# Optimization experiments

Measured on AMD Instinct MI355X. Metric: run time of the kernel, lower is better.

## Reference

```python
import jax, jax.numpy as jnp
import numpy as np

B, T, E, H, D = 2, 2048, 1024, 16, 64  # D = attention_dim // num_heads

def setup_inputs() -> dict:
    key = jax.random.key(0)
    k1, k2, k3, k4 = jax.random.split(key, 4)
    scale = 1.0 / np.sqrt(E)  # ~ torch Linear init scale
    embedded = jax.random.normal(k1, (B, T, E), dtype=jnp.float32)
    Wq = jax.random.normal(k2, (H, D, E), dtype=jnp.float32) * scale
    Wk = jax.random.normal(k3, (H, D, E), dtype=jnp.float32) * scale
    Wv = jax.random.normal(k4, (H, D, E), dtype=jnp.float32) * scale
    return {"embedded": embedded, "Wq": Wq, "Wk": Wk, "Wv": Wv}

def reference(embedded, Wq, Wk, Wv):
    # Batched multi-head projection (original loops per head; same math).
    q = jnp.einsum('bte,hde->bhtd', embedded, Wq)
    k = jnp.einsum('bte,hde->bhtd', embedded, Wk)
    v = jnp.einsum('bte,hde->bhtd', embedded, Wv)
    scores = jnp.einsum('bhtd,bhsd->bhts', q, k) / jnp.sqrt(jnp.float32(D))
    causal = jnp.tril(jnp.ones((T, T), dtype=bool))  # [T,T]
    scores = jnp.where(causal, scores, -jnp.inf)
    attn = jax.nn.softmax(scores, axis=-1)
    out = jnp.einsum('bhts,bhsd->bhtd', attn, v)
    # concat heads on last dim: [B,T,H*D]
    return out.transpose(0, 2, 1, 3).reshape(B, T, H * D)
```

## Files before the change

kernel.cpp:

```cpp
#include <hip/hip_runtime.h>
#include <hip/hip_bf16.h>
#include <stdint.h>

typedef __bf16 bf16_t;
typedef __bf16 bf16x4 __attribute__((ext_vector_type(4)));
typedef __bf16 bf16x8 __attribute__((ext_vector_type(8)));
typedef float  f32x4  __attribute__((ext_vector_type(4)));

#define QK_SCALE 0.1803368801111204f

__device__ __forceinline__ void gload_lds16(const void* g, void* l) {
    __builtin_amdgcn_global_load_lds(
        (__attribute__((address_space(1))) unsigned int*)(uintptr_t)g,
        (__attribute__((address_space(3))) unsigned int*)(uint32_t)(uintptr_t)l,
        16, 0, 0);
}

__global__ __launch_bounds__(256) void convert_kernel(
    const float* __restrict__ emb, const float* __restrict__ wq,
    const float* __restrict__ wk,  const float* __restrict__ wv,
    bf16_t* __restrict__ embb, bf16_t* __restrict__ wcat)
{
    size_t base = ((size_t)blockIdx.x * 256 + threadIdx.x) * 8;
    const float* src;
    bf16_t* dst;
    if (base < (size_t)4194304) { src = emb + base; dst = embb + base; }
    else {
        size_t r = base - 4194304;
        int wsel = (int)(r >> 20);
        size_t off = r & 1048575;
        src = (wsel == 0 ? wq : (wsel == 1 ? wk : wv)) + off;
        dst = wcat + r;
    }
    float4 a  = *(const float4*)src;
    float4 c2 = *(const float4*)(src + 4);
    bf16x8 o;
    o[0]=(bf16_t)a.x;  o[1]=(bf16_t)a.y;  o[2]=(bf16_t)a.z;  o[3]=(bf16_t)a.w;
    o[4]=(bf16_t)c2.x; o[5]=(bf16_t)c2.y; o[6]=(bf16_t)c2.z; o[7]=(bf16_t)c2.w;
    *(bf16x8*)dst = o;
}

__global__ __launch_bounds__(256, 3) void proj_kernel(
    const bf16_t* __restrict__ A, const bf16_t* __restrict__ Wc,
    bf16_t* __restrict__ qo, bf16_t* __restrict__ ko, bf16_t* __restrict__ vto)
{
    __shared__ __align__(128) char smem[49152];

    const int tid  = threadIdx.x;
    const int w    = tid >> 6, lane = tid & 63;
    const int wr   = w >> 1,  wc2  = w & 1;
    const int g    = lane >> 4, c = lane & 15;
    const int bm   = blockIdx.x & 31, bn = blockIdx.x >> 5;
    const int m0   = bm * 128, n0 = bn * 128;

    f32x4 acc[4][4] = {};

    const int arow = lane >> 2;
    const int acol = (((lane & 3) ^ ((lane >> 3) & 3))) * 8;

    #define PROJ_STAGE(buf, kt)                                                        \
        do {                                                                           \
            char* As_ = smem + (buf) * 16384;                                          \
            char* Bs_ = As_ + 8192;                                                    \
            _Pragma("unroll")                                                          \
            for (int p = 0; p < 2; ++p) {                                              \
                gload_lds16(A  + (size_t)(m0 + p*64 + w*16 + arow) * 1024 + (kt)*32 + acol, \
                            As_ + (p*64 + w*16) * 64);                                 \
                gload_lds16(Wc + (size_t)(n0 + p*64 + w*16 + arow) * 1024 + (kt)*32 + acol, \
                            Bs_ + (p*64 + w*16) * 64);                                 \
            }                                                                          \
        } while (0)

    PROJ_STAGE(0, 0);
    PROJ_STAGE(1, 1);
    int cur = 0;
    for (int kt = 0; kt < 32; ++kt) {
        if (kt == 31) asm volatile("s_waitcnt vmcnt(0)" ::: "memory");
        else          asm volatile("s_waitcnt vmcnt(4)" ::: "memory");
        __builtin_amdgcn_s_barrier();
        asm volatile("" ::: "memory");
        if (kt + 2 < 32) {
            int b2 = cur + 2; if (b2 >= 3) b2 -= 3;
            PROJ_STAGE(b2, kt + 2);
        }
        const char* As = smem + cur * 16384;
        const char* Bs = As + 8192;
        const int sw = (c >> 1) & 3;
        bf16x8 af[4], bf[4];
        #pragma unroll
        for (int i = 0; i < 4; ++i) {
            af[i] = *(const bf16x8*)(As + (wr*64  + i*16 + c) * 64 + ((g ^ sw) << 4));
            bf[i] = *(const bf16x8*)(Bs + (wc2*64 + i*16 + c) * 64 + ((g ^ sw) << 4));
        }
        #pragma unroll
        for (int i = 0; i < 4; ++i)
            #pragma unroll
            for (int j = 0; j < 4; ++j)
                acc[i][j] = __builtin_amdgcn_mfma_f32_16x16x32_bf16(af[i], bf[j], acc[i][j], 0, 0, 0);
        cur = (cur == 2) ? 0 : cur + 1;
    }
    __syncthreads();

    const int b  = m0 >> 11;
    const int t0 = m0 & 2047;

    if (n0 < 2048) {
        bf16_t* dst = (n0 < 1024) ? qo : ko;
        const int nl0 = n0 & 1023;
        #pragma unroll
        for (int i = 0; i < 4; ++i)
            #pragma unroll
            for (int j = 0; j < 4; ++j) {
                int dl = wc2*64 + j*16 + c;
                #pragma unroll
                for (int e = 0; e < 4; ++e) {
                    int tl = wr*64 + i*16 + g*4 + e;
                    *(bf16_t*)(smem + ((tl*256 + dl*2) ^ ((tl & 7) << 4))) = (bf16_t)acc[i][j][e];
                }
            }
        __syncthreads();
        #pragma unroll
        for (int it = 0; it < 8; ++it) {
            int chunk = it * 256 + tid;
            int tl = chunk >> 4;
            int ce = (chunk & 15) * 8;
            bf16x8 val = *(const bf16x8*)(smem + ((tl*256 + ce*2) ^ ((tl & 7) << 4)));
            int nn = nl0 + ce;
            int hh = nn >> 6, dd = nn & 63;
            *(bf16x8*)(dst + ((size_t)(b*16 + hh) * 2048 + (t0 + tl)) * 64 + dd) = val;
        }
    } else {
        #pragma unroll
        for (int i = 0; i < 4; ++i)
            #pragma unroll
            for (int j = 0; j < 4; ++j) {
                int dl = wc2*64 + j*16 + c;
                #pragma unroll
                for (int e = 0; e < 4; ++e) {
                    int tl = wr*64 + i*16 + g*4 + e;
                    *(bf16_t*)(smem + ((dl*256 + tl*2) ^ ((dl & 7) << 4))) = (bf16_t)acc[i][j][e];
                }
            }
        __syncthreads();
        const int nvbase = n0 - 2048;
        #pragma unroll
        for (int it = 0; it < 8; ++it) {
            int chunk = it * 256 + tid;
            int dl = chunk >> 4;
            int tc = (chunk & 15) * 8;
            bf16x8 val = *(const bf16x8*)(smem + ((dl*256 + tc*2) ^ ((dl & 7) << 4)));
            int nv = nvbase + dl;
            int hh = nv >> 6, dd = nv & 63;
            *(bf16x8*)(vto + (size_t)((b*16 + hh)*64 + dd) * 2048 + t0 + tc) = val;
        }
    }
    #undef PROJ_STAGE
}

__global__ __launch_bounds__(256, 3) void attn_kernel(
    const bf16_t* __restrict__ qg, const bf16_t* __restrict__ kg,
    const bf16_t* __restrict__ vtg, float* __restrict__ out)
{
    __shared__ __align__(128) char smem[49152];

    const int tid = threadIdx.x;
    const int w = tid >> 6, lane = tid & 63;
    const int g = lane >> 4, c = lane & 15;
    const int id = blockIdx.x;
    const int qt = 31 - (id >> 5);
    const int bh = id & 31;
    const int b = bh >> 4, h = bh & 15;

    const bf16_t* qbase = qg  + (size_t)bh * 2048 * 64;
    const bf16_t* kbase = kg  + (size_t)bh * 2048 * 64;
    const bf16_t* vbase = vtg + (size_t)bh * 64 * 2048;
    float* obase = out + (size_t)b * 2048 * 1024 + h * 64;

    const int srow = lane >> 3;
    const int scol = ((lane & 7) ^ srow) * 8;

    const int q0 = qt * 64;
    const int nt = qt + 1;

    bf16x8 qf[2];
    #pragma unroll
    for (int kf = 0; kf < 2; ++kf) {
        bf16x8 v = *(const bf16x8*)(qbase + (size_t)(q0 + w*16 + c) * 64 + kf*32 + g*8);
        #pragma unroll
        for (int e = 0; e < 8; ++e) qf[kf][e] = (bf16_t)((float)v[e] * QK_SCALE);
    }

    f32x4 oacc[4] = {};
    float mrun = -INFINITY, lrun = 0.0f;

    #define ATTN_STAGE(buf, kt)                                                          \
        do {                                                                             \
            char* Kb_ = smem + (buf) * 16384;                                            \
            _Pragma("unroll")                                                            \
            for (int j = 0; j < 2; ++j) {                                                \
                gload_lds16(kbase + (size_t)((kt)*64 + w*16 + j*8 + srow) * 64 + scol,   \
                            Kb_ + (w*16 + j*8) * 128);                                   \
                gload_lds16(vbase + (size_t)(w*16 + j*8 + srow) * 2048 + (kt)*64 + scol, \
                            Kb_ + 8192 + (w*16 + j*8) * 128);                            \
            }                                                                            \
        } while (0)

    ATTN_STAGE(0, 0);
    if (nt > 1) ATTN_STAGE(1, 1);
    int cur = 0;

    for (int kt = 0; kt < nt; ++kt) {
        if (kt == nt - 1) asm volatile("s_waitcnt vmcnt(0)" ::: "memory");
        else              asm volatile("s_waitcnt vmcnt(4)" ::: "memory");
        __builtin_amdgcn_s_barrier();
        asm volatile("" ::: "memory");
        if (kt + 2 < nt) {
            int b2 = cur + 2; if (b2 >= 3) b2 -= 3;
            ATTN_STAGE(b2, kt + 2);
        }
        const char* Ks = smem + cur * 16384;
        const char* Vs = Ks + 8192;

        f32x4 sacc[4];
        #pragma unroll
        for (int ni = 0; ni < 4; ++ni) {
            int krow = ni*16 + c;
            bf16x8 k0 = *(const bf16x8*)(Ks + krow*128 + ((     g*16) ^ ((c & 7) << 4)));
            bf16x8 k1 = *(const bf16x8*)(Ks + krow*128 + ((64 + g*16) ^ ((c & 7) << 4)));
            f32x4 s0 = {0.f, 0.f, 0.f, 0.f};
            s0 = __builtin_amdgcn_mfma_f32_16x16x32_bf16(k0, qf[0], s0, 0, 0, 0);
            s0 = __builtin_amdgcn_mfma_f32_16x16x32_bf16(k1, qf[1], s0, 0, 0, 0);
            sacc[ni] = s0;
        }

        if (kt == nt - 1) {
            const int qloc = w*16 + c;
            #pragma unroll
            for (int ni = 0; ni < 4; ++ni)
                #pragma unroll
                for (int e = 0; e < 4; ++e)
                    if (ni*16 + g*4 + e > qloc) sacc[ni][e] = -INFINITY;
        }

        float pmax;
        {
            float a0 = fmaxf(fmaxf(sacc[0][0], sacc[0][1]), fmaxf(sacc[0][2], sacc[0][3]));
            float a1 = fmaxf(fmaxf(sacc[1][0], sacc[1][1]), fmaxf(sacc[1][2], sacc[1][3]));
            float a2 = fmaxf(fmaxf(sacc[2][0], sacc[2][1]), fmaxf(sacc[2][2], sacc[2][3]));
            float a3 = fmaxf(fmaxf(sacc[3][0], sacc[3][1]), fmaxf(sacc[3][2], sacc[3][3]));
            pmax = fmaxf(fmaxf(a0, a1), fmaxf(a2, a3));
            pmax = fmaxf(pmax, __shfl_xor(pmax, 16));
            pmax = fmaxf(pmax, __shfl_xor(pmax, 32));
        }

        if (__any(pmax > mrun + 8.0f)) {
            float mnew = fmaxf(mrun, pmax);
            float sc = exp2f(mrun - mnew);
            float s0_ = __shfl(sc, g*4 + 0);
            float s1_ = __shfl(sc, g*4 + 1);
            float s2_ = __shfl(sc, g*4 + 2);
            float s3_ = __shfl(sc, g*4 + 3);
            #pragma unroll
            for (int db = 0; db < 4; ++db) {
                oacc[db][0] *= s0_; oacc[db][1] *= s1_;
                oacc[db][2] *= s2_; oacc[db][3] *= s3_;
            }
            lrun *= sc;
            mrun = mnew;
        }

        float psum = 0.f;
        bf16x8 palo, pahi;
        #pragma unroll
        for (int ni = 0; ni < 4; ++ni)
            #pragma unroll
            for (int e = 0; e < 4; ++e) {
                float pv = exp2f(sacc[ni][e] - mrun);
                psum += pv;
                if (ni < 2) palo[(ni & 1)*4 + e] = (bf16_t)pv;
                else        pahi[(ni & 1)*4 + e] = (bf16_t)pv;
            }
        psum += __shfl_xor(psum, 16);
        psum += __shfl_xor(psum, 32);
        lrun += psum;

        #pragma unroll
        for (int db = 0; db < 4; ++db) {
            int vrow = db*16 + c;
            bf16x4 v0 = *(const bf16x4*)(Vs + vrow*128 + ((     g*8) ^ ((c & 7) << 4)));
            bf16x4 v1 = *(const bf16x4*)(Vs + vrow*128 + ((32 + g*8) ^ ((c & 7) << 4)));
            bf16x4 v2 = *(const bf16x4*)(Vs + vrow*128 + ((64 + g*8) ^ ((c & 7) << 4)));
            bf16x4 v3 = *(const bf16x4*)(Vs + vrow*128 + ((96 + g*8) ^ ((c & 7) << 4)));
            bf16x8 vlo = __builtin_shufflevector(v0, v1, 0, 1, 2, 3, 4, 5, 6, 7);
            bf16x8 vhi = __builtin_shufflevector(v2, v3, 0, 1, 2, 3, 4, 5, 6, 7);
            oacc[db] = __builtin_amdgcn_mfma_f32_16x16x32_bf16(palo, vlo, oacc[db], 0, 0, 0);
            oacc[db] = __builtin_amdgcn_mfma_f32_16x16x32_bf16(pahi, vhi, oacc[db], 0, 0, 0);
        }

        cur = (cur == 2) ? 0 : cur + 1;
    }

    float inv[4];
    #pragma unroll
    for (int e = 0; e < 4; ++e) inv[e] = 1.0f / __shfl(lrun, g*4 + e);
    #pragma unroll
    for (int e = 0; e < 4; ++e) {
        size_t trow = (size_t)(q0 + w*16 + g*4 + e);
        #pragma unroll
        for (int db = 0; db < 4; ++db)
            obase[trow * 1024 + db*16 + c] = oacc[db][e] * inv[e];
    }
    #undef ATTN_STAGE
}

extern "C" void kernel_launch(void* const* d_in, const int* in_sizes, int n_in,
                              void* d_out, int out_size, void* d_ws, size_t ws_size,
                              hipStream_t stream) {
    const float* emb = (const float*)d_in[0];
    const float* wq  = (const float*)d_in[1];
    const float* wk  = (const float*)d_in[2];
    const float* wv  = (const float*)d_in[3];
    float* out = (float*)d_out;

    char* ws = (char*)d_ws;
    bf16_t* embb = (bf16_t*)ws;
    bf16_t* wcat = (bf16_t*)(ws + (size_t) 8*1024*1024);
    bf16_t* qb   = (bf16_t*)(ws + (size_t)14*1024*1024);
    bf16_t* kb   = (bf16_t*)(ws + (size_t)22*1024*1024);
    bf16_t* vtb  = (bf16_t*)(ws + (size_t)30*1024*1024);

    convert_kernel<<<3584, 256, 0, stream>>>(emb, wq, wk, wv, embb, wcat);
    proj_kernel<<<768, 256, 0, stream>>>(embb, wcat, qb, kb, vtb);
    attn_kernel<<<1024, 256, 0, stream>>>(qb, kb, vtb, out);
}
```

Measured before the change: 154.4 us.

## Use 128-row query tiles with 8 waves, permute V layout, add MFMA priority

The attention kernel now runs 512-thread blocks that each cover 128 query rows (8 waves), so each K/V tile staged in LDS is shared by twice as many waves, and the grid shrinks to 512 blocks with a balanced qt ordering. The projection kernel writes V^T with a permuted token order, so the attention kernel can read a V fragment with two 16-byte LDS loads instead of four 8-byte loads. s_setprio is placed around the MFMA sections, the row-sum shuffles are moved after the PV MFMAs, and the max reduction is reshaped. The risks are that the new V permutation and masking offsets must match exactly for correctness, and that larger blocks may reduce scheduling flexibility.

Result: faster. 151.3 us (-2.1%).

```diff
diff --git a/kernel.cpp b/kernel.cpp
--- a/kernel.cpp
+++ b/kernel.cpp
@@ -92,11 +92,13 @@
             af[i] = *(const bf16x8*)(As + (wr*64  + i*16 + c) * 64 + ((g ^ sw) << 4));
             bf[i] = *(const bf16x8*)(Bs + (wc2*64 + i*16 + c) * 64 + ((g ^ sw) << 4));
         }
+        __builtin_amdgcn_s_setprio(1);
         #pragma unroll
         for (int i = 0; i < 4; ++i)
             #pragma unroll
             for (int j = 0; j < 4; ++j)
                 acc[i][j] = __builtin_amdgcn_mfma_f32_16x16x32_bf16(af[i], bf[j], acc[i][j], 0, 0, 0);
+        __builtin_amdgcn_s_setprio(0);
         cur = (cur == 2) ? 0 : cur + 1;
     }
     __syncthreads();
@@ -147,17 +149,22 @@
         for (int it = 0; it < 8; ++it) {
             int chunk = it * 256 + tid;
             int dl = chunk >> 4;
-            int tc = (chunk & 15) * 8;
-            bf16x8 val = *(const bf16x8*)(smem + ((dl*256 + tc*2) ^ ((dl & 7) << 4)));
+            int tl = (chunk & 15) * 8;
+            int B64 = tl >> 6;
+            int r   = tl & 63;
+            int t_a = B64*64 + ((r >> 3) & 1) * 32 + (r >> 4) * 4;
+            bf16x4 lo = *(const bf16x4*)(smem + ((dl*256 + t_a*2)      ^ ((dl & 7) << 4)));
+            bf16x4 hi = *(const bf16x4*)(smem + ((dl*256 + (t_a+16)*2) ^ ((dl & 7) << 4)));
+            bf16x8 val = __builtin_shufflevector(lo, hi, 0, 1, 2, 3, 4, 5, 6, 7);
             int nv = nvbase + dl;
             int hh = nv >> 6, dd = nv & 63;
-            *(bf16x8*)(vto + (size_t)((b*16 + hh)*64 + dd) * 2048 + t0 + tc) = val;
+            *(bf16x8*)(vto + (size_t)((b*16 + hh)*64 + dd) * 2048 + t0 + tl) = val;
         }
     }
     #undef PROJ_STAGE
 }
 
-__global__ __launch_bounds__(256, 3) void attn_kernel(
+__global__ __launch_bounds__(512, 4) void attn_kernel(
     const bf16_t* __restrict__ qg, const bf16_t* __restrict__ kg,
     const bf16_t* __restrict__ vtg, float* __restrict__ out)
 {
@@ -167,7 +174,8 @@
     const int w = tid >> 6, lane = tid & 63;
     const int g = lane >> 4, c = lane & 15;
     const int id = blockIdx.x;
-    const int qt = 31 - (id >> 5);
+    const int j = id >> 5;
+    const int qt = (j < 8) ? (15 - j) : (j - 8);
     const int bh = id & 31;
     const int b = bh >> 4, h = bh & 15;
 
@@ -179,8 +187,8 @@
     const int srow = lane >> 3;
     const int scol = ((lane & 7) ^ srow) * 8;
 
-    const int q0 = qt * 64;
-    const int nt = qt + 1;
+    const int q0 = qt * 128;
+    const int nt = 2 * qt + 2;
 
     bf16x8 qf[2];
     #pragma unroll
@@ -193,25 +201,22 @@
     f32x4 oacc[4] = {};
     float mrun = -INFINITY, lrun = 0.0f;
 
-    #define ATTN_STAGE(buf, kt)                                                          \
-        do {                                                                             \
-            char* Kb_ = smem + (buf) * 16384;                                            \
-            _Pragma("unroll")                                                            \
-            for (int j = 0; j < 2; ++j) {                                                \
-                gload_lds16(kbase + (size_t)((kt)*64 + w*16 + j*8 + srow) * 64 + scol,   \
-                            Kb_ + (w*16 + j*8) * 128);                                   \
-                gload_lds16(vbase + (size_t)(w*16 + j*8 + srow) * 2048 + (kt)*64 + scol, \
-                            Kb_ + 8192 + (w*16 + j*8) * 128);                            \
-            }                                                                            \
+    #define ATTN_STAGE(buf, kt)                                                        \
+        do {                                                                           \
+            char* Kb_ = smem + (buf) * 16384;                                          \
+            gload_lds16(kbase + (size_t)((kt)*64 + w*8 + srow) * 64 + scol,            \
+                        Kb_ + w*1024);                                                 \
+            gload_lds16(vbase + (size_t)(w*8 + srow) * 2048 + (kt)*64 + scol,          \
+                        Kb_ + 8192 + w*1024);                                          \
         } while (0)
 
     ATTN_STAGE(0, 0);
-    if (nt > 1) ATTN_STAGE(1, 1);
+    ATTN_STAGE(1, 1);
     int cur = 0;
 
     for (int kt = 0; kt < nt; ++kt) {
         if (kt == nt - 1) asm volatile("s_waitcnt vmcnt(0)" ::: "memory");
-        else              asm volatile("s_waitcnt vmcnt(4)" ::: "memory");
+        else              asm volatile("s_waitcnt vmcnt(2)" ::: "memory");
         __builtin_amdgcn_s_barrier();
         asm volatile("" ::: "memory");
         if (kt + 2 < nt) {
@@ -222,6 +227,7 @@
         const char* Vs = Ks + 8192;
 
         f32x4 sacc[4];
+        __builtin_amdgcn_s_setprio(1);
         #pragma unroll
         for (int ni = 0; ni < 4; ++ni) {
             int krow = ni*16 + c;
@@ -232,23 +238,28 @@
             s0 = __builtin_amdgcn_mfma_f32_16x16x32_bf16(k1, qf[1], s0, 0, 0, 0);
             sacc[ni] = s0;
         }
-
-        if (kt == nt - 1) {
+        __builtin_amdgcn_s_setprio(0);
+
+        if (kt >= nt - 2) {
             const int qloc = w*16 + c;
+            const int koff = (kt - (nt - 2)) * 64;
             #pragma unroll
             for (int ni = 0; ni < 4; ++ni)
                 #pragma unroll
                 for (int e = 0; e < 4; ++e)
-                    if (ni*16 + g*4 + e > qloc) sacc[ni][e] = -INFINITY;
+                    if (koff + ni*16 + g*4 + e > qloc) sacc[ni][e] = -INFINITY;
         }
 
         float pmax;
         {
-            float a0 = fmaxf(fmaxf(sacc[0][0], sacc[0][1]), fmaxf(sacc[0][2], sacc[0][3]));
-            float a1 = fmaxf(fmaxf(sacc[1][0], sacc[1][1]), fmaxf(sacc[1][2], sacc[1][3]));
-            float a2 = fmaxf(fmaxf(sacc[2][0], sacc[2][1]), fmaxf(sacc[2][2], sacc[2][3]));
-            float a3 = fmaxf(fmaxf(sacc[3][0], sacc[3][1]), fmaxf(sacc[3][2], sacc[3][3]));
-            pmax = fmaxf(fmaxf(a0, a1), fmaxf(a2, a3));
+            float t0_ = fmaxf(fmaxf(sacc[0][0], sacc[0][1]), sacc[0][2]);
+            float t1_ = fmaxf(fmaxf(sacc[0][3], sacc[1][0]), sacc[1][1]);
+            float t2_ = fmaxf(fmaxf(sacc[1][2], sacc[1][3]), sacc[2][0]);
+            float t3_ = fmaxf(fmaxf(sacc[2][1], sacc[2][2]), sacc[2][3]);
+            float t4_ = fmaxf(fmaxf(sacc[3][0], sacc[3][1]), sacc[3][2]);
+            float u_  = fmaxf(fmaxf(t0_, t1_), t2_);
+            float v_  = fmaxf(fmaxf(t3_, t4_), sacc[3][3]);
+            pmax = fmaxf(u_, v_);
             pmax = fmaxf(pmax, __shfl_xor(pmax, 16));
             pmax = fmaxf(pmax, __shfl_xor(pmax, 32));
         }
@@ -280,22 +291,21 @@
                 if (ni < 2) palo[(ni & 1)*4 + e] = (bf16_t)pv;
                 else        pahi[(ni & 1)*4 + e] = (bf16_t)pv;
             }
+
+        __builtin_amdgcn_s_setprio(1);
+        #pragma unroll
+        for (int db = 0; db < 4; ++db) {
+            int vrow = db*16 + c;
+            bf16x8 vlo = *(const bf16x8*)(Vs + vrow*128 + ((g*32     ) ^ ((c & 7) << 4)));
+            bf16x8 vhi = *(const bf16x8*)(Vs + vrow*128 + ((g*32 + 16) ^ ((c & 7) << 4)));
+            oacc[db] = __builtin_amdgcn_mfma_f32_16x16x32_bf16(palo, vlo, oacc[db], 0, 0, 0);
+            oacc[db] = __builtin_amdgcn_mfma_f32_16x16x32_bf16(pahi, vhi, oacc[db], 0, 0, 0);
+        }
+        __builtin_amdgcn_s_setprio(0);
+
         psum += __shfl_xor(psum, 16);
         psum += __shfl_xor(psum, 32);
         lrun += psum;
-
-        #pragma unroll
-        for (int db = 0; db < 4; ++db) {
-            int vrow = db*16 + c;
-            bf16x4 v0 = *(const bf16x4*)(Vs + vrow*128 + ((     g*8) ^ ((c & 7) << 4)));
-            bf16x4 v1 = *(const bf16x4*)(Vs + vrow*128 + ((32 + g*8) ^ ((c & 7) << 4)));
-            bf16x4 v2 = *(const bf16x4*)(Vs + vrow*128 + ((64 + g*8) ^ ((c & 7) << 4)));
-            bf16x4 v3 = *(const bf16x4*)(Vs + vrow*128 + ((96 + g*8) ^ ((c & 7) << 4)));
-            bf16x8 vlo = __builtin_shufflevector(v0, v1, 0, 1, 2, 3, 4, 5, 6, 7);
-            bf16x8 vhi = __builtin_shufflevector(v2, v3, 0, 1, 2, 3, 4, 5, 6, 7);
-            oacc[db] = __builtin_amdgcn_mfma_f32_16x16x32_bf16(palo, vlo, oacc[db], 0, 0, 0);
-            oacc[db] = __builtin_amdgcn_mfma_f32_16x16x32_bf16(pahi, vhi, oacc[db], 0, 0, 0);
-        }
 
         cur = (cur == 2) ? 0 : cur + 1;
     }
@@ -331,5 +341,5 @@
 
     convert_kernel<<<3584, 256, 0, stream>>>(emb, wq, wk, wv, embb, wcat);
     proj_kernel<<<768, 256, 0, stream>>>(embb, wcat, qb, kb, vtb);
-    attn_kernel<<<1024, 256, 0, stream>>>(qb, kb, vtb, out);
-}
+    attn_kernel<<<512, 512, 0, stream>>>(qb, kb, vtb, out);
+}
```
